# Kernel optimization log

Hardware: AMD Instinct MI355X
Metric: run time of the kernel (lower is better)

The kernel has to match this reference:

```python
import jax, jax.numpy as jnp
import numpy as np

BETA_MIN = 0.1
BETA_MAX = 20.0


def _Beta(t):
    # integral of linear beta schedule
    return BETA_MIN * t + 0.5 * (BETA_MAX - BETA_MIN) * t ** 2


def setup_inputs() -> dict:
    key = jax.random.key(0)
    k1, k2, k3, k4, k5 = jax.random.split(key, 5)
    B, K, D = 4096, 128, 256
    x = jax.random.normal(k1, (B, D), dtype=jnp.float32)
    t = jax.random.uniform(k2, (B,), dtype=jnp.float32)
    centers = jax.random.normal(k3, (K, D), dtype=jnp.float32)
    # keep stds positive and well-conditioned
    stds = 0.5 + 0.5 * jax.random.uniform(k4, (K, D), dtype=jnp.float32)
    # positive mixture weights (original only requires positivity, takes log)
    weights = 0.1 + jax.random.uniform(k5, (K,), dtype=jnp.float32)
    return {"x": x, "t": t, "centers": centers, "stds": stds, "weights": weights}


def reference(x, t, centers, stds, weights):
    ndim = centers.shape[1]

    def log_prob(xx):
        Bt = _Beta(t)[:, None, None]                 # [B,1,1]
        a = jnp.exp(-Bt / 2)
        centers_t = a * centers[None]                # [B,K,D]
        var_t = jnp.exp(-Bt) * stds[None] ** 2 + 1.0 - jnp.exp(-Bt)  # [B,K,D]
        diff = xx[:, None, :] - centers_t            # [B,K,D]
        # NOTE: faithful to source, which uses ndim/2 * sum(log(2*pi*var)) (not 1/2)
        lp = (-(diff ** 2) / (2.0 * var_t)).sum(-1) \
             - (ndim / 2) * jnp.log(2.0 * jnp.pi * var_t).sum(-1)    # [B,K]
        lp = lp + jnp.log(weights)[None, :]
        return jax.scipy.special.logsumexp(lp, axis=1)               # [B]

    grad_log_prob = jax.grad(lambda xx: log_prob(xx).sum())(x)       # [B,D]
    Bt = _Beta(t)[:, None]                                           # [B,1]
    return -jnp.sqrt(1.0 - jnp.exp(-Bt)) * grad_log_prob
```

## Files before the change

kernel.cpp:

```cpp
#include <hip/hip_runtime.h>
#include <math.h>


constexpr int Kc = 128;
constexpr int Dc = 256;
constexpr int G  = 4;

typedef float f4 __attribute__((ext_vector_type(4)));

__global__ void prep_kernel(const float* __restrict__ centers,
                            const float* __restrict__ stds,
                            float* __restrict__ CT4, float* __restrict__ AT4) {
    int idx = blockIdx.x * blockDim.x + threadIdx.x;
    if (idx >= Kc * Dc) return;
    int k = idx >> 8;
    int d = idx & (Dc - 1);
    int o = (d >> 2) * (Kc * 4) + k * 4 + (d & 3);
    float c = centers[idx];
    float s = stds[idx];
    CT4[o] = c;
    AT4[o] = s * s - 1.0f;
}

__global__ __launch_bounds__(256) void score_kernel(
    const float* __restrict__ x, const float* __restrict__ t,
    const float* __restrict__ centers, const float* __restrict__ stds,
    const float* __restrict__ weights,
    const float* __restrict__ CT4, const float* __restrict__ AT4,
    float* __restrict__ out)
{
    const int b0  = blockIdx.x * G;
    const int tid = threadIdx.x;

    __shared__ __align__(16) float xT[Dc][G];
    __shared__ float part1[G][2][Kc];
    __shared__ float partL[G][2][Kc];
    __shared__ __align__(16) float peT[Kc][G];
    __shared__ float wmax[G][2];
    __shared__ float wsum[G][2];

    float e[G], na[G], onee[G], sg[G];
    #pragma unroll
    for (int g = 0; g < G; ++g) {
        float tt = t[b0 + g];
        float Bt = fmaf(9.95f * tt, tt, 0.1f * tt);
        float ee = __expf(-Bt);
        e[g]    = ee;
        na[g]   = -sqrtf(ee);
        onee[g] = 1.0f - ee;
        sg[g]   = sqrtf(1.0f - ee);
    }

    #pragma unroll
    for (int g = 0; g < G; ++g)
        xT[tid][g] = x[(b0 + g) * Dc + tid];
    __syncthreads();

    const int kk    = tid & (Kc - 1);
    const int half  = tid >> 7;
    const int dbase = half * (Dc / 2);

    const f4* CT4v = (const f4*)CT4;
    const f4* AT4v = (const f4*)AT4;
    const f4* xTv  = (const f4*)(&xT[0][0]);

    float acc1[G] = {0.f, 0.f, 0.f, 0.f};
    float accL[G] = {0.f, 0.f, 0.f, 0.f};

    for (int grp = 0; grp < 8; ++grp) {
        float prod[G] = {1.f, 1.f, 1.f, 1.f};
        #pragma unroll
        for (int q = 0; q < 4; ++q) {
            const int d0 = dbase + (grp * 4 + q) * 4;
            const int qi = (d0 >> 2) * Kc + kk;
            f4 c4  = CT4v[qi];
            f4 A4  = AT4v[qi];
            f4 xv0 = xTv[d0 + 0];
            f4 xv1 = xTv[d0 + 1];
            f4 xv2 = xTv[d0 + 2];
            f4 xv3 = xTv[d0 + 3];
            #pragma unroll
            for (int g = 0; g < G; ++g) {
                float v0 = fmaf(e[g], A4[0], 1.0f);
                float v1 = fmaf(e[g], A4[1], 1.0f);
                float v2 = fmaf(e[g], A4[2], 1.0f);
                float v3 = fmaf(e[g], A4[3], 1.0f);
                float f0 = fmaf(na[g], c4[0], xv0[g]);
                float f1 = fmaf(na[g], c4[1], xv1[g]);
                float f2 = fmaf(na[g], c4[2], xv2[g]);
                float f3 = fmaf(na[g], c4[3], xv3[g]);
                float s0 = f0 * f0, s1 = f1 * f1, s2 = f2 * f2, s3 = f3 * f3;
                float d01 = v0 * v1, d23 = v2 * v3;
                float n01 = s0 * v1; n01 = fmaf(s1, v0, n01);
                float n23 = s2 * v3; n23 = fmaf(s3, v2, n23);
                float den = d01 * d23;
                float num = n01 * d23; num = fmaf(n23, d01, num);
                acc1[g] = fmaf(num, __builtin_amdgcn_rcpf(den), acc1[g]);
                prod[g] *= den;
            }
        }
        #pragma unroll
        for (int g = 0; g < G; ++g)
            accL[g] += __log2f(prod[g]);
    }
    #pragma unroll
    for (int g = 0; g < G; ++g) {
        part1[g][half][kk] = acc1[g];
        partL[g][half][kk] = accL[g];
    }
    __syncthreads();

    float lpv[G];
    if (tid < Kc) {
        float lw = __logf(weights[tid]);
        #pragma unroll
        for (int g = 0; g < G; ++g) {
            float S1 = part1[g][0][tid] + part1[g][1][tid];
            float S2 = partL[g][0][tid] + partL[g][1][tid];
            lpv[g] = fmaf(-0.5f, S1, fmaf(-88.72283911167299f, S2, lw));
            float m = lpv[g];
            #pragma unroll
            for (int off = 32; off > 0; off >>= 1)
                m = fmaxf(m, __shfl_xor(m, off, 64));
            if ((tid & 63) == 0) wmax[g][tid >> 6] = m;
        }
    }
    __syncthreads();
    if (tid < Kc) {
        #pragma unroll
        for (int g = 0; g < G; ++g) {
            float m  = fmaxf(wmax[g][0], wmax[g][1]);
            float pe = __expf(lpv[g] - m);
            peT[tid][g] = pe;
            float s = pe;
            #pragma unroll
            for (int off = 32; off > 0; off >>= 1)
                s += __shfl_xor(s, off, 64);
            if ((tid & 63) == 0) wsum[g][tid >> 6] = s;
        }
    }
    __syncthreads();

    f4 xvv = xTv[tid];
    float O[G] = {0.f, 0.f, 0.f, 0.f};
    const f4* peTv = (const f4*)(&peT[0][0]);
    const float* cp = centers + tid;
    const float* sp = stds + tid;

    for (int kq = 0; kq < 32; ++kq) {
        const int k0 = kq * 4;
        float c0 = cp[(k0 + 0) * Dc];
        float c1 = cp[(k0 + 1) * Dc];
        float c2 = cp[(k0 + 2) * Dc];
        float c3 = cp[(k0 + 3) * Dc];
        float t0 = sp[(k0 + 0) * Dc];
        float t1 = sp[(k0 + 1) * Dc];
        float t2 = sp[(k0 + 2) * Dc];
        float t3 = sp[(k0 + 3) * Dc];
        f4 p0 = peTv[k0 + 0];
        f4 p1 = peTv[k0 + 1];
        f4 p2 = peTv[k0 + 2];
        f4 p3 = peTv[k0 + 3];
        float s20 = t0 * t0, s21 = t1 * t1, s22 = t2 * t2, s23 = t3 * t3;
        #pragma unroll
        for (int g = 0; g < G; ++g) {
            float v0 = fmaf(e[g], s20, onee[g]);
            float v1 = fmaf(e[g], s21, onee[g]);
            float v2 = fmaf(e[g], s22, onee[g]);
            float v3 = fmaf(e[g], s23, onee[g]);
            float f0 = fmaf(na[g], c0, xvv[g]);
            float f1 = fmaf(na[g], c1, xvv[g]);
            float f2 = fmaf(na[g], c2, xvv[g]);
            float f3 = fmaf(na[g], c3, xvv[g]);
            float u0 = p0[g] * f0;
            float u1 = p1[g] * f1;
            float u2 = p2[g] * f2;
            float u3 = p3[g] * f3;
            float d01 = v0 * v1, d23 = v2 * v3;
            float n01 = u0 * v1; n01 = fmaf(u1, v0, n01);
            float n23 = u2 * v3; n23 = fmaf(u3, v2, n23);
            float den = d01 * d23;
            float num = n01 * d23; num = fmaf(n23, d01, num);
            O[g] = fmaf(num, __builtin_amdgcn_rcpf(den), O[g]);
        }
    }

    #pragma unroll
    for (int g = 0; g < G; ++g) {
        float Z = wsum[g][0] + wsum[g][1];
        out[(b0 + g) * Dc + tid] = sg[g] * __builtin_amdgcn_rcpf(Z) * O[g];
    }
}

extern "C" void kernel_launch(void* const* d_in, const int* in_sizes, int n_in,
                              void* d_out, int out_size, void* d_ws, size_t ws_size,
                              hipStream_t stream) {
    const float* x       = (const float*)d_in[0];
    const float* t       = (const float*)d_in[1];
    const float* centers = (const float*)d_in[2];
    const float* stds    = (const float*)d_in[3];
    const float* weights = (const float*)d_in[4];
    float* outp = (float*)d_out;

    float* CT4 = (float*)d_ws;
    float* AT4 = CT4 + Kc * Dc;

    const int B = in_sizes[1];

    prep_kernel<<<(Kc * Dc + 255) / 256, 256, 0, stream>>>(centers, stds, CT4, AT4);
    score_kernel<<<B / G, 256, 0, stream>>>(x, t, centers, stds, weights, CT4, AT4, outp);
}
```

Measured before the change: 114.9 us.

## Use packed float2 math and interleaved center/variance layouts in score kernel

Rewrites both inner loops to work on pairs of batch rows with two-wide float vectors, so the compiler can emit packed FMA/MUL instructions (v_pk_fma_f32) on MI355X. The prep kernel now interleaves centers and s^2-1 into one 8-float record per (d-quad, k) and also writes a (c, A) pair array, so each phase does a single contiguous load stream and the second phase no longer squares stds. It also adds a launch_bounds occupancy hint of 6 blocks. Risks include extra lane-shuffle moves to assemble the packed operands and register pressure from the occupancy cap.

```diff
diff --git a/kernel.cpp b/kernel.cpp
--- a/kernel.cpp
+++ b/kernel.cpp
@@ -6,27 +6,34 @@
 constexpr int Dc = 256;
 constexpr int G  = 4;
 
+typedef float f2 __attribute__((ext_vector_type(2)));
 typedef float f4 __attribute__((ext_vector_type(4)));
+
+static __device__ __forceinline__ f2 fma2(f2 a, f2 b, f2 c) {
+    return __builtin_elementwise_fma(a, b, c);
+}
+static __device__ __forceinline__ f2 splat2(float s) { return (f2){s, s}; }
 
 __global__ void prep_kernel(const float* __restrict__ centers,
                             const float* __restrict__ stds,
-                            float* __restrict__ CT4, float* __restrict__ AT4) {
+                            float* __restrict__ CA8, f2* __restrict__ P2) {
     int idx = blockIdx.x * blockDim.x + threadIdx.x;
     if (idx >= Kc * Dc) return;
     int k = idx >> 8;
     int d = idx & (Dc - 1);
-    int o = (d >> 2) * (Kc * 4) + k * 4 + (d & 3);
     float c = centers[idx];
     float s = stds[idx];
-    CT4[o] = c;
-    AT4[o] = s * s - 1.0f;
-}
-
-__global__ __launch_bounds__(256) void score_kernel(
+    float A = s * s - 1.0f;
+    int o = (d >> 2) * (Kc * 8) + k * 8 + (d & 3);
+    CA8[o]     = c;
+    CA8[o + 4] = A;
+    P2[idx] = (f2){c, A};
+}
+
+__global__ __launch_bounds__(256, 6) void score_kernel(
     const float* __restrict__ x, const float* __restrict__ t,
-    const float* __restrict__ centers, const float* __restrict__ stds,
     const float* __restrict__ weights,
-    const float* __restrict__ CT4, const float* __restrict__ AT4,
+    const float* __restrict__ CA8, const f2* __restrict__ P2,
     float* __restrict__ out)
 {
     const int b0  = blockIdx.x * G;
@@ -39,17 +46,19 @@
     __shared__ float wmax[G][2];
     __shared__ float wsum[G][2];
 
-    float e[G], na[G], onee[G], sg[G];
+    float e[G], na[G], sg[G];
     #pragma unroll
     for (int g = 0; g < G; ++g) {
         float tt = t[b0 + g];
         float Bt = fmaf(9.95f * tt, tt, 0.1f * tt);
         float ee = __expf(-Bt);
-        e[g]    = ee;
-        na[g]   = -sqrtf(ee);
-        onee[g] = 1.0f - ee;
-        sg[g]   = sqrtf(1.0f - ee);
-    }
+        e[g]  = ee;
+        na[g] = -sqrtf(ee);
+        sg[g] = sqrtf(1.0f - ee);
+    }
+    f2 e2[2]  = {{e[0], e[1]}, {e[2], e[3]}};
+    f2 na2[2] = {{na[0], na[1]}, {na[2], na[3]}};
+    const f2 one2 = {1.0f, 1.0f};
 
     #pragma unroll
     for (int g = 0; g < G; ++g)
@@ -60,54 +69,63 @@
     const int half  = tid >> 7;
     const int dbase = half * (Dc / 2);
 
-    const f4* CT4v = (const f4*)CT4;
-    const f4* AT4v = (const f4*)AT4;
-    const f4* xTv  = (const f4*)(&xT[0][0]);
-
-    float acc1[G] = {0.f, 0.f, 0.f, 0.f};
+    const f4* xTv = (const f4*)(&xT[0][0]);
+
+    f2 acc1[2] = {{0.f, 0.f}, {0.f, 0.f}};
     float accL[G] = {0.f, 0.f, 0.f, 0.f};
 
     for (int grp = 0; grp < 8; ++grp) {
-        float prod[G] = {1.f, 1.f, 1.f, 1.f};
+        f2 prod[2] = {{1.f, 1.f}, {1.f, 1.f}};
         #pragma unroll
         for (int q = 0; q < 4; ++q) {
             const int d0 = dbase + (grp * 4 + q) * 4;
-            const int qi = (d0 >> 2) * Kc + kk;
-            f4 c4  = CT4v[qi];
-            f4 A4  = AT4v[qi];
+            const float* base = CA8 + ((size_t)(d0 >> 2) * Kc + kk) * 8;
+            f4 c4 = *(const f4*)base;
+            f4 A4 = *(const f4*)(base + 4);
             f4 xv0 = xTv[d0 + 0];
             f4 xv1 = xTv[d0 + 1];
             f4 xv2 = xTv[d0 + 2];
             f4 xv3 = xTv[d0 + 3];
             #pragma unroll
-            for (int g = 0; g < G; ++g) {
-                float v0 = fmaf(e[g], A4[0], 1.0f);
-                float v1 = fmaf(e[g], A4[1], 1.0f);
-                float v2 = fmaf(e[g], A4[2], 1.0f);
-                float v3 = fmaf(e[g], A4[3], 1.0f);
-                float f0 = fmaf(na[g], c4[0], xv0[g]);
-                float f1 = fmaf(na[g], c4[1], xv1[g]);
-                float f2 = fmaf(na[g], c4[2], xv2[g]);
-                float f3 = fmaf(na[g], c4[3], xv3[g]);
-                float s0 = f0 * f0, s1 = f1 * f1, s2 = f2 * f2, s3 = f3 * f3;
-                float d01 = v0 * v1, d23 = v2 * v3;
-                float n01 = s0 * v1; n01 = fmaf(s1, v0, n01);
-                float n23 = s2 * v3; n23 = fmaf(s3, v2, n23);
-                float den = d01 * d23;
-                float num = n01 * d23; num = fmaf(n23, d01, num);
-                acc1[g] = fmaf(num, __builtin_amdgcn_rcpf(den), acc1[g]);
-                prod[g] *= den;
+            for (int p = 0; p < 2; ++p) {
+                f2 ep = e2[p], nap = na2[p];
+                f2 x0 = {xv0[2*p], xv0[2*p+1]};
+                f2 x1 = {xv1[2*p], xv1[2*p+1]};
+                f2 x2 = {xv2[2*p], xv2[2*p+1]};
+                f2 x3 = {xv3[2*p], xv3[2*p+1]};
+                f2 v0 = fma2(ep, splat2(A4[0]), one2);
+                f2 v1 = fma2(ep, splat2(A4[1]), one2);
+                f2 v2 = fma2(ep, splat2(A4[2]), one2);
+                f2 v3 = fma2(ep, splat2(A4[3]), one2);
+                f2 f0 = fma2(nap, splat2(c4[0]), x0);
+                f2 f1 = fma2(nap, splat2(c4[1]), x1);
+                f2 f2_ = fma2(nap, splat2(c4[2]), x2);
+                f2 f3 = fma2(nap, splat2(c4[3]), x3);
+                f2 s0 = f0 * f0, s1 = f1 * f1, s2 = f2_ * f2_, s3 = f3 * f3;
+                f2 d01 = v0 * v1, d23 = v2 * v3;
+                f2 n01 = fma2(s1, v0, s0 * v1);
+                f2 n23 = fma2(s3, v2, s2 * v3);
+                f2 den = d01 * d23;
+                f2 num = fma2(n23, d01, n01 * d23);
+                f2 r = {__builtin_amdgcn_rcpf(den[0]),
+                        __builtin_amdgcn_rcpf(den[1])};
+                acc1[p] = fma2(num, r, acc1[p]);
+                prod[p] = prod[p] * den;
             }
         }
-        #pragma unroll
-        for (int g = 0; g < G; ++g)
-            accL[g] += __log2f(prod[g]);
-    }
-    #pragma unroll
-    for (int g = 0; g < G; ++g) {
-        part1[g][half][kk] = acc1[g];
+        accL[0] += __log2f(prod[0][0]);
+        accL[1] += __log2f(prod[0][1]);
+        accL[2] += __log2f(prod[1][0]);
+        accL[3] += __log2f(prod[1][1]);
+    }
+    #pragma unroll
+    for (int p = 0; p < 2; ++p) {
+        part1[2*p  ][half][kk] = acc1[p][0];
+        part1[2*p+1][half][kk] = acc1[p][1];
+    }
+    #pragma unroll
+    for (int g = 0; g < G; ++g)
         partL[g][half][kk] = accL[g];
-    }
     __syncthreads();
 
     float lpv[G];
@@ -142,53 +160,55 @@
     __syncthreads();
 
     f4 xvv = xTv[tid];
-    float O[G] = {0.f, 0.f, 0.f, 0.f};
+    f2 xp[2] = {{xvv[0], xvv[1]}, {xvv[2], xvv[3]}};
+    f2 O[2] = {{0.f, 0.f}, {0.f, 0.f}};
     const f4* peTv = (const f4*)(&peT[0][0]);
-    const float* cp = centers + tid;
-    const float* sp = stds + tid;
+    const f2* pp = P2 + tid;
 
     for (int kq = 0; kq < 32; ++kq) {
         const int k0 = kq * 4;
-        float c0 = cp[(k0 + 0) * Dc];
-        float c1 = cp[(k0 + 1) * Dc];
-        float c2 = cp[(k0 + 2) * Dc];
-        float c3 = cp[(k0 + 3) * Dc];
-        float t0 = sp[(k0 + 0) * Dc];
-        float t1 = sp[(k0 + 1) * Dc];
-        float t2 = sp[(k0 + 2) * Dc];
-        float t3 = sp[(k0 + 3) * Dc];
+        f2 ca0 = pp[(k0 + 0) * Dc];
+        f2 ca1 = pp[(k0 + 1) * Dc];
+        f2 ca2 = pp[(k0 + 2) * Dc];
+        f2 ca3 = pp[(k0 + 3) * Dc];
         f4 p0 = peTv[k0 + 0];
         f4 p1 = peTv[k0 + 1];
         f4 p2 = peTv[k0 + 2];
         f4 p3 = peTv[k0 + 3];
-        float s20 = t0 * t0, s21 = t1 * t1, s22 = t2 * t2, s23 = t3 * t3;
-        #pragma unroll
-        for (int g = 0; g < G; ++g) {
-            float v0 = fmaf(e[g], s20, onee[g]);
-            float v1 = fmaf(e[g], s21, onee[g]);
-            float v2 = fmaf(e[g], s22, onee[g]);
-            float v3 = fmaf(e[g], s23, onee[g]);
-            float f0 = fmaf(na[g], c0, xvv[g]);
-            float f1 = fmaf(na[g], c1, xvv[g]);
-            float f2 = fmaf(na[g], c2, xvv[g]);
-            float f3 = fmaf(na[g], c3, xvv[g]);
-            float u0 = p0[g] * f0;
-            float u1 = p1[g] * f1;
-            float u2 = p2[g] * f2;
-            float u3 = p3[g] * f3;
-            float d01 = v0 * v1, d23 = v2 * v3;
-            float n01 = u0 * v1; n01 = fmaf(u1, v0, n01);
-            float n23 = u2 * v3; n23 = fmaf(u3, v2, n23);
-            float den = d01 * d23;
-            float num = n01 * d23; num = fmaf(n23, d01, num);
-            O[g] = fmaf(num, __builtin_amdgcn_rcpf(den), O[g]);
-        }
-    }
-
-    #pragma unroll
-    for (int g = 0; g < G; ++g) {
-        float Z = wsum[g][0] + wsum[g][1];
-        out[(b0 + g) * Dc + tid] = sg[g] * __builtin_amdgcn_rcpf(Z) * O[g];
+        #pragma unroll
+        for (int p = 0; p < 2; ++p) {
+            f2 ep = e2[p], nap = na2[p];
+            f2 v0 = fma2(ep, splat2(ca0[1]), one2);
+            f2 v1 = fma2(ep, splat2(ca1[1]), one2);
+            f2 v2 = fma2(ep, splat2(ca2[1]), one2);
+            f2 v3 = fma2(ep, splat2(ca3[1]), one2);
+            f2 f0 = fma2(nap, splat2(ca0[0]), xp[p]);
+            f2 f1 = fma2(nap, splat2(ca1[0]), xp[p]);
+            f2 f2_ = fma2(nap, splat2(ca2[0]), xp[p]);
+            f2 f3 = fma2(nap, splat2(ca3[0]), xp[p]);
+            f2 u0 = (f2){p0[2*p], p0[2*p+1]} * f0;
+            f2 u1 = (f2){p1[2*p], p1[2*p+1]} * f1;
+            f2 u2 = (f2){p2[2*p], p2[2*p+1]} * f2_;
+            f2 u3 = (f2){p3[2*p], p3[2*p+1]} * f3;
+            f2 d01 = v0 * v1, d23 = v2 * v3;
+            f2 n01 = fma2(u1, v0, u0 * v1);
+            f2 n23 = fma2(u3, v2, u2 * v3);
+            f2 den = d01 * d23;
+            f2 num = fma2(n23, d01, n01 * d23);
+            f2 r = {__builtin_amdgcn_rcpf(den[0]),
+                    __builtin_amdgcn_rcpf(den[1])};
+            O[p] = fma2(num, r, O[p]);
+        }
+    }
+
+    #pragma unroll
+    for (int p = 0; p < 2; ++p) {
+        #pragma unroll
+        for (int j = 0; j < 2; ++j) {
+            int g = 2 * p + j;
+            float Z = wsum[g][0] + wsum[g][1];
+            out[(b0 + g) * Dc + tid] = sg[g] * __builtin_amdgcn_rcpf(Z) * O[p][j];
+        }
     }
 }
 
@@ -202,11 +222,11 @@
     const float* weights = (const float*)d_in[4];
     float* outp = (float*)d_out;
 
-    float* CT4 = (float*)d_ws;
-    float* AT4 = CT4 + Kc * Dc;
+    float* CA8 = (float*)d_ws;
+    f2*    P2  = (f2*)(CA8 + Kc * Dc * 2);
 
     const int B = in_sizes[1];
 
-    prep_kernel<<<(Kc * Dc + 255) / 256, 256, 0, stream>>>(centers, stds, CT4, AT4);
-    score_kernel<<<B / G, 256, 0, stream>>>(x, t, centers, stds, weights, CT4, AT4, outp);
-}
+    prep_kernel<<<(Kc * Dc + 255) / 256, 256, 0, stream>>>(centers, stds, CA8, P2);
+    score_kernel<<<B / G, 256, 0, stream>>>(x, t, weights, CA8, P2, outp);
+}
```

Result: faster. 102.1 us (-11.2%).
